# Optimization experiments

Measured on AMD Instinct MI355X. Metric: run time of the kernel, lower is better.

Reference implementation:

```python
import jax, jax.numpy as jnp
import numpy as np

# Model dims (match init_kwargs)
H = 16        # num query heads
HKV = 4       # num key/value heads
D = 128       # head dim
HID = H * D   # hidden size = 2048
W = 4         # ring world size; we simulate rank W-1 (sees all kv shards)
SL = 2048     # local (per-rank) sequence length


def _block_attn(q, kb, vb, scale, causal):
    # q: [B,H,Sl,D], kb/vb: [B,H,Sl,D]
    S = jnp.einsum('bhqd,bhkd->bhqk', q, kb) * scale
    if causal:
        mask = jnp.triu(jnp.ones((q.shape[2], kb.shape[2]), dtype=bool), k=1)
        S = jnp.where(mask[None, None], -jnp.inf, S)
    S_max = jnp.max(S, axis=-1, keepdims=True)
    exp_S = jnp.exp(S - S_max)
    exp_sum = jnp.sum(exp_S, axis=-1, keepdims=True)
    lse = jnp.log(exp_sum) + S_max            # [B,H,Sl,1]
    O = jnp.einsum('bhqk,bhkd->bhqd', exp_S / exp_sum, vb)
    return O, lse


def _ring_attention_fwd(x_q, x_kv, Wq, Wk, Wv, Wo):
    B, Sl, hid = x_q.shape
    n_rep = H // HKV
    scale = 1.0 / np.sqrt(D).astype(np.float32)

    q = (x_q @ Wq.T).reshape(B, Sl, H, D).transpose(0, 2, 1, 3)          # [B,H,Sl,D]
    k = (x_kv @ Wk.T).reshape(B, -1, HKV, D).transpose(0, 2, 1, 3)       # [B,Hkv,Stot,D]
    v = (x_kv @ Wv.T).reshape(B, -1, HKV, D).transpose(0, 2, 1, 3)
    # repeat_kv (GQA)
    k = jnp.repeat(k, n_rep, axis=1)                                     # [B,H,Stot,D]
    v = jnp.repeat(v, n_rep, axis=1)
    # split kv into W ring shards along sequence
    kb = k.reshape(B, H, W, Sl, D)
    vb = v.reshape(B, H, W, Sl, D)

    out, lse = None, None
    rank = W - 1
    for step in range(W):  # fixed small ring loop
        blk = rank - step  # shard held at this ring step (own shard first)
        bo, blse = _block_attn(q, kb[:, :, blk], vb[:, :, blk], scale, causal=(step == 0))
        if out is None:
            out, lse = bo, blse
        else:
            # online merge (matches update_out_and_lse)
            out = out - jax.nn.sigmoid(blse - lse) * (out - bo)
            lse = lse - jax.nn.log_sigmoid(lse - blse)

    out = out.transpose(0, 2, 1, 3).reshape(B, Sl, H * D)
    return out @ Wo.T


def setup_inputs() -> dict:
    key = jax.random.key(0)
    ks = jax.random.split(key, 6)
    s = 0.02
    return {
        'x_q': jax.random.normal(ks[0], (1, SL, HID), dtype=jnp.float32),
        'x_kv': jax.random.normal(ks[1], (1, W * SL, HID), dtype=jnp.float32),
        'Wq': jax.random.normal(ks[2], (HID, HID), dtype=jnp.float32) * s,
        'Wk': jax.random.normal(ks[3], (HKV * D, HID), dtype=jnp.float32) * s,
        'Wv': jax.random.normal(ks[4], (HKV * D, HID), dtype=jnp.float32) * s,
        'Wo': jax.random.normal(ks[5], (HID, HID), dtype=jnp.float32) * s,
    }


def reference(x_q, x_kv, Wq, Wk, Wv, Wo):
    return _ring_attention_fwd(x_q, x_kv, Wq, Wk, Wv, Wo)
```

## Files before the change

### kernel.cpp

```cpp
#include <hip/hip_runtime.h>
#include <stdint.h>

typedef unsigned short u16;
typedef short bf16x8 __attribute__((ext_vector_type(8)));
typedef float f32x4 __attribute__((ext_vector_type(4)));

#define MFMA16(a, b, c) __builtin_amdgcn_mfma_f32_16x16x32_bf16(a, b, c, 0, 0, 0)

__device__ __forceinline__ void ld_lds16(const void* g, void* l) {
  __builtin_amdgcn_global_load_lds(
      (const __attribute__((address_space(1))) void*)(uint64_t)(uintptr_t)g,
      (__attribute__((address_space(3))) void*)(uint32_t)(uintptr_t)l,
      16, 0, 0);
}

__device__ __forceinline__ u16 f32_to_bf16(float f) {
  uint32_t u = __float_as_uint(f);
  return (u16)((u + 0x7FFFu + ((u >> 16) & 1u)) >> 16);
}

__device__ __forceinline__ uint32_t cvt_pk_bf16(float a, float b) {
  uint32_t r;
  asm("v_cvt_pk_bf16_f32 %0, %1, %2" : "=v"(r) : "v"(a), "v"(b));
  return r;
}

__global__ void cvt_all(const float* __restrict__ xq, const float* __restrict__ xkv,
                        const float* __restrict__ Wq, const float* __restrict__ Wk,
                        const float* __restrict__ Wv, const float* __restrict__ Wo,
                        u16* __restrict__ xq_b, u16* __restrict__ xkv_b,
                        u16* __restrict__ wq_b, u16* __restrict__ wk_b,
                        u16* __restrict__ wv_b, u16* __restrict__ wo_b) {
  const int M4 = 1 << 20;
  const int total = 7 * M4 + (M4 >> 1);
  int i = blockIdx.x * blockDim.x + threadIdx.x;
  int stride = gridDim.x * blockDim.x;
  for (; i < total; i += stride) {
    const float* src;
    u16* dst;
    int off;
    if (i < M4)                         { src = xq;  dst = xq_b;  off = i; }
    else if (i < 5 * M4)                { src = xkv; dst = xkv_b; off = i - M4; }
    else if (i < 6 * M4)                { src = Wq;  dst = wq_b;  off = i - 5 * M4; }
    else if (i < 6 * M4 + (M4 >> 2))    { src = Wk;  dst = wk_b;  off = i - 6 * M4; }
    else if (i < 6 * M4 + (M4 >> 1))    { src = Wv;  dst = wv_b;  off = i - 6 * M4 - (M4 >> 2); }
    else                                { src = Wo;  dst = wo_b;  off = i - 6 * M4 - (M4 >> 1); }
    float4 v = reinterpret_cast<const float4*>(src)[off];
    ushort4 o;
    o.x = f32_to_bf16(v.x); o.y = f32_to_bf16(v.y);
    o.z = f32_to_bf16(v.z); o.w = f32_to_bf16(v.w);
    reinterpret_cast<ushort4*>(dst)[off] = o;
  }
}

__device__ __forceinline__ void gemm_body(const u16* __restrict__ A,
                                          const u16* __restrict__ B,
                                          void* __restrict__ Cv, int M, int N,
                                          int K, float alpha, int bx, int by,
                                          int outf32, u16* lA, u16* lB) {
  const int tid = threadIdx.x;
  const int lane = tid & 63;
  const int w = tid >> 6;
  const int c = lane & 15, g = lane >> 4;
  const int wm = (w & 1) * 64, wn = (w >> 1) * 32;
  const int m0 = by * 128, n0 = bx * 64;
  const int sr = tid >> 3, sc = tid & 7;

  f32x4 acc[4][2] = {};

  for (int k0 = 0; k0 < K; k0 += 64) {
    __syncthreads();
#pragma unroll
    for (int p = 0; p < 4; ++p) {
      int row = p * 32 + sr;
      int gc = sc ^ (row & 7);
      ld_lds16(A + (size_t)(m0 + row) * K + k0 + gc * 8, &lA[row * 64 + sc * 8]);
    }
#pragma unroll
    for (int p = 0; p < 2; ++p) {
      int idx = p * 256 + tid;
      int row = idx >> 3, cc = idx & 7;
      int gc = cc ^ (row & 7);
      ld_lds16(B + (size_t)(n0 + row) * K + k0 + gc * 8, &lB[row * 64 + cc * 8]);
    }
    __syncthreads();
#pragma unroll
    for (int kc = 0; kc < 2; ++kc) {
      bf16x8 a[4], b[2];
#pragma unroll
      for (int t = 0; t < 4; ++t) {
        int row = wm + t * 16 + c;
        int ch = (g + 4 * kc) ^ (row & 7);
        a[t] = *(const bf16x8*)&lA[row * 64 + ch * 8];
      }
#pragma unroll
      for (int t = 0; t < 2; ++t) {
        int row = wn + t * 16 + c;
        int ch = (g + 4 * kc) ^ (row & 7);
        b[t] = *(const bf16x8*)&lB[row * 64 + ch * 8];
      }
#pragma unroll
      for (int i = 0; i < 4; ++i)
#pragma unroll
        for (int j = 0; j < 2; ++j)
          acc[i][j] = MFMA16(a[i], b[j], acc[i][j]);
    }
  }

#pragma unroll
  for (int i = 0; i < 4; ++i)
#pragma unroll
    for (int j = 0; j < 2; ++j)
#pragma unroll
      for (int r = 0; r < 4; ++r) {
        int mm = m0 + wm + i * 16 + g * 4 + r;
        int nn = n0 + wn + j * 16 + c;
        float v = acc[i][j][r] * alpha;
        if (outf32)
          ((float*)Cv)[(size_t)mm * N + nn] = v;
        else
          ((u16*)Cv)[(size_t)mm * N + nn] = f32_to_bf16(v);
      }
}

__global__ __launch_bounds__(256, 4)
void gemm3(const u16* __restrict__ xq_b, const u16* __restrict__ wq_b,
           u16* __restrict__ Qb, const u16* __restrict__ xkv_b,
           const u16* __restrict__ wk_b, u16* __restrict__ Kb,
           const u16* __restrict__ wv_b, u16* __restrict__ VTb, float qscale) {
  __shared__ u16 lA[128 * 64];
  __shared__ u16 lB[64 * 64];
  int b = blockIdx.x;
  if (b < 512) {
    gemm_body(xq_b, wq_b, Qb, 2048, 2048, 2048, qscale, b & 31, b >> 5, 0, lA, lB);
  } else if (b < 1024) {
    b -= 512;
    gemm_body(xkv_b, wk_b, Kb, 8192, 512, 2048, 1.0f, b & 7, b >> 3, 0, lA, lB);
  } else {
    b -= 1024;
    gemm_body(wv_b, xkv_b, VTb, 512, 8192, 2048, 1.0f, b & 127, b >> 7, 0, lA, lB);
  }
}

__global__ __launch_bounds__(256, 4)
void gemm_out(const u16* __restrict__ A, const u16* __restrict__ B,
              float* __restrict__ Cv) {
  __shared__ u16 lA[128 * 64];
  __shared__ u16 lB[64 * 64];
  gemm_body(A, B, Cv, 2048, 2048, 2048, 1.0f, blockIdx.x, blockIdx.y, 1, lA, lB);
}

__global__ __launch_bounds__(256, 2)
void attn_kernel(const u16* __restrict__ Q, const u16* __restrict__ Kg,
                 const u16* __restrict__ VT, float* __restrict__ Opart,
                 float* __restrict__ mlp) {
  __shared__ u16 lK[2][64 * 128];
  __shared__ u16 lV[2][128 * 64];
  __shared__ uint32_t lP32[4][16 * 36];

  const int tid = threadIdx.x;
  const int w = tid >> 6, lane = tid & 63;
  const int c = lane & 15, g = lane >> 4;
  const int bx = blockIdx.x;
  const int h = bx & 15, kvs = bx >> 8;
  const int qbr = (bx >> 4) & 15;
  const int qb = kvs ? qbr : 15 - qbr;
  const int hk = h >> 2;
  const int i0 = qb * 128;
  const int q0 = i0 + w * 32;

  const int nt = ((i0 + 6271) >> 6) + 1;
  const int nth = nt >> 1;
  const int t0 = kvs ? nth : 0;
  const int ntt = (kvs ? nt : nth) - t0;

  bf16x8 qf0[4], qf1[4];
#pragma unroll
  for (int kc = 0; kc < 4; ++kc) {
    qf0[kc] = *(const bf16x8*)&Q[(size_t)(q0 + c) * 2048 + h * 128 + kc * 32 + g * 8];
    qf1[kc] = *(const bf16x8*)&Q[(size_t)(q0 + 16 + c) * 2048 + h * 128 + kc * 32 + g * 8];
  }

  bf16x8 onesf;
#pragma unroll
  for (int i = 0; i < 8; ++i) onesf[i] = (short)0x3F80;

  f32x4 a0[8] = {}, a1[8] = {};
  f32x4 lacc0 = {}, lacc1 = {};

  auto stage = [&](int buf, int t) {
    const int j0 = t << 6;
#pragma unroll
    for (int p = 0; p < 4; ++p) {
      int idx = p * 256 + tid;
      int row = idx >> 4, cc = idx & 15;
      int gc = cc ^ (row & 15);
      ld_lds16(Kg + (size_t)(j0 + row) * 512 + hk * 128 + gc * 8,
               &lK[buf][row * 128 + cc * 8]);
    }
#pragma unroll
    for (int p = 0; p < 4; ++p) {
      int idx = p * 256 + tid;
      int row = idx >> 3, cc = idx & 7;
      int gc = cc ^ (row & 7);
      ld_lds16(VT + (size_t)(hk * 128 + row) * 8192 + j0 + gc * 8,
               &lV[buf][row * 64 + cc * 8]);
    }
  };

  uint32_t* lPw = &lP32[w][0];

  auto softmax_pb = [&](f32x4 (&sm)[4], bf16x8 (&pb)[2]) {
#pragma unroll
    for (int jt = 0; jt < 4; ++jt) {
      lPw[c * 36 + jt * 8 + g * 2 + 0] =
          cvt_pk_bf16(exp2f(sm[jt][0]), exp2f(sm[jt][1]));
      lPw[c * 36 + jt * 8 + g * 2 + 1] =
          cvt_pk_bf16(exp2f(sm[jt][2]), exp2f(sm[jt][3]));
    }
    pb[0] = *(const bf16x8*)&lPw[c * 36 + g * 4];
    pb[1] = *(const bf16x8*)&lPw[c * 36 + 16 + g * 4];
  };

  stage(0, t0);

  for (int it = 0; it < ntt; ++it) {
    const int curb = it & 1;
    const int j0 = (t0 + it) << 6;
    if (it + 1 < ntt) {
      stage(curb ^ 1, t0 + it + 1);
      asm volatile("s_waitcnt vmcnt(8)" ::: "memory");
    } else {
      asm volatile("s_waitcnt vmcnt(0)" ::: "memory");
    }
    __builtin_amdgcn_s_barrier();

    f32x4 s0[4] = {}, s1[4] = {};
    __builtin_amdgcn_s_setprio(1);
#pragma unroll
    for (int kc = 0; kc < 4; ++kc)
#pragma unroll
      for (int jt = 0; jt < 4; ++jt) {
        int row = jt * 16 + c;
        int ch = (g + 4 * kc) ^ (row & 15);
        bf16x8 kf = *(const bf16x8*)&lK[curb][row * 128 + ch * 8];
        s0[jt] = MFMA16(kf, qf0[kc], s0[jt]);
        s1[jt] = MFMA16(kf, qf1[kc], s1[jt]);
      }
    __builtin_amdgcn_s_setprio(0);

    if (j0 + 63 > q0 + 6144) {
#pragma unroll
      for (int jt = 0; jt < 4; ++jt)
#pragma unroll
        for (int r = 0; r < 4; ++r) {
          int jg = j0 + jt * 16 + g * 4 + r;
          if (jg > q0 + c + 6144) s0[jt][r] = -1e30f;
          if (jg > q0 + 16 + c + 6144) s1[jt][r] = -1e30f;
        }
    }

    bf16x8 pb0[2], pb1[2];
    softmax_pb(s0, pb0);
    softmax_pb(s1, pb1);

    __builtin_amdgcn_s_setprio(1);
    lacc0 = MFMA16(onesf, pb0[0], lacc0);
    lacc0 = MFMA16(onesf, pb0[1], lacc0);
    lacc1 = MFMA16(onesf, pb1[0], lacc1);
    lacc1 = MFMA16(onesf, pb1[1], lacc1);
#pragma unroll
    for (int dt = 0; dt < 8; ++dt)
#pragma unroll
      for (int kc2 = 0; kc2 < 2; ++kc2) {
        int row = dt * 16 + c;
        int vch = (g + 4 * kc2) ^ (row & 7);
        bf16x8 vf = *(const bf16x8*)&lV[curb][row * 64 + vch * 8];
        a0[dt] = MFMA16(vf, pb0[kc2], a0[dt]);
        a1[dt] = MFMA16(vf, pb1[kc2], a1[dt]);
      }
    __builtin_amdgcn_s_setprio(0);

    __builtin_amdgcn_s_barrier();
  }

  const size_t pbase = ((size_t)(kvs * 16 + h) * 16 + qb);
  float* Op = Opart + pbase * 16384;
  float* mlb = mlp + pbase * 256;
  const int qi0 = w * 32 + c;
#pragma unroll
  for (int dt = 0; dt < 8; ++dt) {
    *(f32x4*)&Op[(size_t)qi0 * 128 + dt * 16 + g * 4] = a0[dt];
    *(f32x4*)&Op[(size_t)(qi0 + 16) * 128 + dt * 16 + g * 4] = a1[dt];
  }
  if (g == 0) {
    mlb[128 + qi0] = lacc0[0];
    mlb[128 + qi0 + 16] = lacc1[0];
  }
}

__global__ __launch_bounds__(256)
void attn_merge(const float* __restrict__ Opart, const float* __restrict__ mlp,
                u16* __restrict__ O) {
  const int bx = blockIdx.x;
  const int h = bx >> 4, qb = bx & 15;
  const int q = threadIdx.x & 127, hf = threadIdx.x >> 7;
  const size_t p0 = ((size_t)(0 + h) * 16 + qb);
  const size_t p1 = ((size_t)(16 + h) * 16 + qb);
  float ll0 = mlp[p0 * 256 + 128 + q], ll1 = mlp[p1 * 256 + 128 + q];
  float inv = 1.f / (ll0 + ll1);
  const float* A = Opart + p0 * 16384 + (size_t)q * 128 + hf * 64;
  const float* B = Opart + p1 * 16384 + (size_t)q * 128 + hf * 64;
  u16* out = O + (size_t)(qb * 128 + q) * 2048 + h * 128 + hf * 64;
#pragma unroll
  for (int d = 0; d < 64; d += 4) {
    float4 a = *(const float4*)&A[d];
    float4 b = *(const float4*)&B[d];
    ushort4 o;
    o.x = f32_to_bf16((a.x + b.x) * inv);
    o.y = f32_to_bf16((a.y + b.y) * inv);
    o.z = f32_to_bf16((a.z + b.z) * inv);
    o.w = f32_to_bf16((a.w + b.w) * inv);
    *(ushort4*)&out[d] = o;
  }
}

extern "C" void kernel_launch(void* const* d_in, const int* in_sizes, int n_in,
                              void* d_out, int out_size, void* d_ws, size_t ws_size,
                              hipStream_t stream) {
  (void)in_sizes; (void)n_in; (void)out_size; (void)ws_size;
  const float* xq = (const float*)d_in[0];
  const float* xkv = (const float*)d_in[1];
  const float* Wq = (const float*)d_in[2];
  const float* Wk = (const float*)d_in[3];
  const float* Wv = (const float*)d_in[4];
  const float* Wo = (const float*)d_in[5];

  u16* ws = (u16*)d_ws;
  const size_t M1 = 1024 * 1024;
  u16* xq_b  = ws;
  u16* xkv_b = ws + 4 * M1;
  u16* wq_b  = ws + 20 * M1;
  u16* wk_b  = ws + 24 * M1;
  u16* wv_b  = ws + 25 * M1;
  u16* wo_b  = ws + 26 * M1;
  u16* Qb    = ws + 30 * M1;
  u16* Kb    = ws + 34 * M1;
  u16* VTb   = ws + 38 * M1;
  u16* Ob    = ws + 42 * M1;
  float* Opart = (float*)d_ws;
  float* mlptr = Opart + 8388608;

  cvt_all<<<2048, 256, 0, stream>>>(xq, xkv, Wq, Wk, Wv, Wo,
                                    xq_b, xkv_b, wq_b, wk_b, wv_b, wo_b);

  gemm3<<<1536, 256, 0, stream>>>(xq_b, wq_b, Qb, xkv_b, wk_b, Kb, wv_b, VTb,
                                  0.12752837f);

  attn_kernel<<<512, 256, 0, stream>>>(Qb, Kb, VTb, Opart, mlptr);
  attn_merge<<<256, 256, 0, stream>>>(Opart, mlptr, Ob);

  gemm_out<<<dim3(32, 16), 256, 0, stream>>>(Ob, wo_b, (float*)d_out);
}
```

Measured before the change: 295.8 us.

## Switch attention kernel to 32x32x16 MFMA with in-register P permute

Rewrites the attention inner loop to use 32x32x16 bf16 MFMAs instead of 16x16x32. The softmax probabilities now stay in registers and are rearranged into the PV operand layout with v_permlane32_swap, replacing the LDS round trip through lP32. The row sum is computed with VALU adds and a cross-half shuffle rather than extra MFMAs against a ones vector. The output store becomes scalar per-element writes, which may coalesce less well than the previous vector stores.

```diff
diff --git a/kernel.cpp b/kernel.cpp
--- a/kernel.cpp
+++ b/kernel.cpp
@@ -4,8 +4,10 @@
 typedef unsigned short u16;
 typedef short bf16x8 __attribute__((ext_vector_type(8)));
 typedef float f32x4 __attribute__((ext_vector_type(4)));
+typedef float f32x16 __attribute__((ext_vector_type(16)));
 
 #define MFMA16(a, b, c) __builtin_amdgcn_mfma_f32_16x16x32_bf16(a, b, c, 0, 0, 0)
+#define MFMA32(a, b, c) __builtin_amdgcn_mfma_f32_32x32x16_bf16(a, b, c, 0, 0, 0)
 
 __device__ __forceinline__ void ld_lds16(const void* g, void* l) {
   __builtin_amdgcn_global_load_lds(
@@ -23,6 +25,10 @@
   uint32_t r;
   asm("v_cvt_pk_bf16_f32 %0, %1, %2" : "=v"(r) : "v"(a), "v"(b));
   return r;
+}
+
+__device__ __forceinline__ void perm_swap(uint32_t& x, uint32_t& y) {
+  asm volatile("v_permlane32_swap_b32 %0, %1" : "+v"(x), "+v"(y));
 }
 
 __global__ void cvt_all(const float* __restrict__ xq, const float* __restrict__ xkv,
@@ -156,11 +162,10 @@
                  float* __restrict__ mlp) {
   __shared__ u16 lK[2][64 * 128];
   __shared__ u16 lV[2][128 * 64];
-  __shared__ uint32_t lP32[4][16 * 36];
 
   const int tid = threadIdx.x;
   const int w = tid >> 6, lane = tid & 63;
-  const int c = lane & 15, g = lane >> 4;
+  const int ql = lane & 31, hi = lane >> 5;
   const int bx = blockIdx.x;
   const int h = bx & 15, kvs = bx >> 8;
   const int qbr = (bx >> 4) & 15;
@@ -174,19 +179,13 @@
   const int t0 = kvs ? nth : 0;
   const int ntt = (kvs ? nt : nth) - t0;
 
-  bf16x8 qf0[4], qf1[4];
-#pragma unroll
-  for (int kc = 0; kc < 4; ++kc) {
-    qf0[kc] = *(const bf16x8*)&Q[(size_t)(q0 + c) * 2048 + h * 128 + kc * 32 + g * 8];
-    qf1[kc] = *(const bf16x8*)&Q[(size_t)(q0 + 16 + c) * 2048 + h * 128 + kc * 32 + g * 8];
-  }
-
-  bf16x8 onesf;
-#pragma unroll
-  for (int i = 0; i < 8; ++i) onesf[i] = (short)0x3F80;
-
-  f32x4 a0[8] = {}, a1[8] = {};
-  f32x4 lacc0 = {}, lacc1 = {};
+  bf16x8 qf[8];
+#pragma unroll
+  for (int kc = 0; kc < 8; ++kc)
+    qf[kc] = *(const bf16x8*)&Q[(size_t)(q0 + ql) * 2048 + h * 128 + kc * 16 + hi * 8];
+
+  f32x16 a[4] = {};
+  float ls = 0.f;
 
   auto stage = [&](int buf, int t) {
     const int j0 = t << 6;
@@ -206,20 +205,6 @@
       ld_lds16(VT + (size_t)(hk * 128 + row) * 8192 + j0 + gc * 8,
                &lV[buf][row * 64 + cc * 8]);
     }
-  };
-
-  uint32_t* lPw = &lP32[w][0];
-
-  auto softmax_pb = [&](f32x4 (&sm)[4], bf16x8 (&pb)[2]) {
-#pragma unroll
-    for (int jt = 0; jt < 4; ++jt) {
-      lPw[c * 36 + jt * 8 + g * 2 + 0] =
-          cvt_pk_bf16(exp2f(sm[jt][0]), exp2f(sm[jt][1]));
-      lPw[c * 36 + jt * 8 + g * 2 + 1] =
-          cvt_pk_bf16(exp2f(sm[jt][2]), exp2f(sm[jt][3]));
-    }
-    pb[0] = *(const bf16x8*)&lPw[c * 36 + g * 4];
-    pb[1] = *(const bf16x8*)&lPw[c * 36 + 16 + g * 4];
   };
 
   stage(0, t0);
@@ -235,49 +220,78 @@
     }
     __builtin_amdgcn_s_barrier();
 
-    f32x4 s0[4] = {}, s1[4] = {};
+    f32x16 s0 = {}, s1 = {};
     __builtin_amdgcn_s_setprio(1);
 #pragma unroll
+    for (int kc = 0; kc < 8; ++kc) {
+      int ch = kc * 2 + hi;
+      bf16x8 kfa = *(const bf16x8*)&lK[curb][ql * 128 + (ch ^ (ql & 15)) * 8];
+      bf16x8 kfb = *(const bf16x8*)&lK[curb][(32 + ql) * 128 + (ch ^ (ql & 15)) * 8];
+      s0 = MFMA32(kfa, qf[kc], s0);
+      s1 = MFMA32(kfb, qf[kc], s1);
+    }
+    __builtin_amdgcn_s_setprio(0);
+
+    if (j0 + 63 > q0 + 6144) {
+#pragma unroll
+      for (int r = 0; r < 16; ++r) {
+        int jrow = (r & 3) + 8 * (r >> 2) + 4 * hi;
+        if (j0 + jrow > q0 + ql + 6144) s0[r] = -1e30f;
+        if (j0 + 32 + jrow > q0 + ql + 6144) s1[r] = -1e30f;
+      }
+    }
+
+    float t0s = 0.f, t1s = 0.f, t2s = 0.f, t3s = 0.f;
+#pragma unroll
+    for (int r = 0; r < 16; r += 4) {
+      s0[r] = exp2f(s0[r]);     t0s += s0[r];
+      s0[r + 1] = exp2f(s0[r + 1]); t1s += s0[r + 1];
+      s0[r + 2] = exp2f(s0[r + 2]); t2s += s0[r + 2];
+      s0[r + 3] = exp2f(s0[r + 3]); t3s += s0[r + 3];
+    }
+#pragma unroll
+    for (int r = 0; r < 16; r += 4) {
+      s1[r] = exp2f(s1[r]);     t0s += s1[r];
+      s1[r + 1] = exp2f(s1[r + 1]); t1s += s1[r + 1];
+      s1[r + 2] = exp2f(s1[r + 2]); t2s += s1[r + 2];
+      s1[r + 3] = exp2f(s1[r + 3]); t3s += s1[r + 3];
+    }
+    float ts = (t0s + t1s) + (t2s + t3s);
+    ts += __shfl_xor(ts, 32);
+    ls += ts;
+
+    bf16x8 pbf[4];
+#pragma unroll
+    for (int jt = 0; jt < 2; ++jt) {
+      const f32x16& sv = jt ? s1 : s0;
+      uint32_t A0 = cvt_pk_bf16(sv[0], sv[1]);
+      uint32_t B0 = cvt_pk_bf16(sv[4], sv[5]);
+      perm_swap(A0, B0);
+      uint32_t A1 = cvt_pk_bf16(sv[2], sv[3]);
+      uint32_t B1 = cvt_pk_bf16(sv[6], sv[7]);
+      perm_swap(A1, B1);
+      uint32_t A2 = cvt_pk_bf16(sv[8], sv[9]);
+      uint32_t B2 = cvt_pk_bf16(sv[12], sv[13]);
+      perm_swap(A2, B2);
+      uint32_t A3 = cvt_pk_bf16(sv[10], sv[11]);
+      uint32_t B3 = cvt_pk_bf16(sv[14], sv[15]);
+      perm_swap(A3, B3);
+      union { uint32_t u[4]; bf16x8 v; } pa, pb;
+      pa.u[0] = A0; pa.u[1] = A1; pa.u[2] = B0; pa.u[3] = B1;
+      pb.u[0] = A2; pb.u[1] = A3; pb.u[2] = B2; pb.u[3] = B3;
+      pbf[2 * jt] = pa.v;
+      pbf[2 * jt + 1] = pb.v;
+    }
+
+    __builtin_amdgcn_s_setprio(1);
+#pragma unroll
     for (int kc = 0; kc < 4; ++kc)
 #pragma unroll
-      for (int jt = 0; jt < 4; ++jt) {
-        int row = jt * 16 + c;
-        int ch = (g + 4 * kc) ^ (row & 15);
-        bf16x8 kf = *(const bf16x8*)&lK[curb][row * 128 + ch * 8];
-        s0[jt] = MFMA16(kf, qf0[kc], s0[jt]);
-        s1[jt] = MFMA16(kf, qf1[kc], s1[jt]);
-      }
-    __builtin_amdgcn_s_setprio(0);
-
-    if (j0 + 63 > q0 + 6144) {
-#pragma unroll
-      for (int jt = 0; jt < 4; ++jt)
-#pragma unroll
-        for (int r = 0; r < 4; ++r) {
-          int jg = j0 + jt * 16 + g * 4 + r;
-          if (jg > q0 + c + 6144) s0[jt][r] = -1e30f;
-          if (jg > q0 + 16 + c + 6144) s1[jt][r] = -1e30f;
-        }
-    }
-
-    bf16x8 pb0[2], pb1[2];
-    softmax_pb(s0, pb0);
-    softmax_pb(s1, pb1);
-
-    __builtin_amdgcn_s_setprio(1);
-    lacc0 = MFMA16(onesf, pb0[0], lacc0);
-    lacc0 = MFMA16(onesf, pb0[1], lacc0);
-    lacc1 = MFMA16(onesf, pb1[0], lacc1);
-    lacc1 = MFMA16(onesf, pb1[1], lacc1);
-#pragma unroll
-    for (int dt = 0; dt < 8; ++dt)
-#pragma unroll
-      for (int kc2 = 0; kc2 < 2; ++kc2) {
-        int row = dt * 16 + c;
-        int vch = (g + 4 * kc2) ^ (row & 7);
-        bf16x8 vf = *(const bf16x8*)&lV[curb][row * 64 + vch * 8];
-        a0[dt] = MFMA16(vf, pb0[kc2], a0[dt]);
-        a1[dt] = MFMA16(vf, pb1[kc2], a1[dt]);
+      for (int dt = 0; dt < 4; ++dt) {
+        int row = dt * 32 + ql;
+        int ch = (kc * 2 + hi) ^ (row & 7);
+        bf16x8 vf = *(const bf16x8*)&lV[curb][row * 64 + ch * 8];
+        a[dt] = MFMA32(pbf[kc], vf, a[dt]);
       }
     __builtin_amdgcn_s_setprio(0);
 
@@ -287,16 +301,14 @@
   const size_t pbase = ((size_t)(kvs * 16 + h) * 16 + qb);
   float* Op = Opart + pbase * 16384;
   float* mlb = mlp + pbase * 256;
-  const int qi0 = w * 32 + c;
-#pragma unroll
-  for (int dt = 0; dt < 8; ++dt) {
-    *(f32x4*)&Op[(size_t)qi0 * 128 + dt * 16 + g * 4] = a0[dt];
-    *(f32x4*)&Op[(size_t)(qi0 + 16) * 128 + dt * 16 + g * 4] = a1[dt];
-  }
-  if (g == 0) {
-    mlb[128 + qi0] = lacc0[0];
-    mlb[128 + qi0 + 16] = lacc1[0];
-  }
+#pragma unroll
+  for (int dt = 0; dt < 4; ++dt)
+#pragma unroll
+    for (int r = 0; r < 16; ++r) {
+      int qrow = w * 32 + (r & 3) + 8 * (r >> 2) + 4 * hi;
+      Op[(size_t)qrow * 128 + dt * 32 + ql] = a[dt][r];
+    }
+  if (hi == 0) mlb[128 + w * 32 + ql] = ls;
 }
 
 __global__ __launch_bounds__(256)
```

Measured after the change: 296.9 us. No clear change (+0.4%).
